# Optimization experiments

Hardware: AMD Instinct MI355X
Metric: run time of the kernel (lower is better)

## Reference

```python
import jax, jax.numpy as jnp
import numpy as np

N = 8192
F_IN, F1, F2 = 11, 16, 32
HEADS = 3
D_CAT = 2 * F2          # 64, concat of interface + neighborhood branches
D_POOL = D_CAT * HEADS  # 192


def setup_inputs() -> dict:
    key = jax.random.key(0)
    ks = jax.random.split(key, 16)
    s = 0.1
    return {
        "x_int": jax.random.normal(ks[0], (N, F_IN), jnp.float32),
        "x_nh": jax.random.normal(ks[1], (N, F_IN), jnp.float32),
        # dense soft adjacencies, scaled ~1/N so aggregates stay O(1)
        "adj_int": jax.random.uniform(ks[2], (N, N), jnp.float32) / N,
        "adj_nh": jax.random.uniform(ks[3], (N, N), jnp.float32) / N,
        "W1_int": jax.random.normal(ks[4], (F_IN, F1), jnp.float32) * s,
        "b1_int": jnp.zeros((F1,), jnp.float32),
        "W1_nh": jax.random.normal(ks[5], (F_IN, F1), jnp.float32) * s,
        "b1_nh": jnp.zeros((F1,), jnp.float32),
        "W2_int": jax.random.normal(ks[6], (F1, F2), jnp.float32) * s,
        "b2_int": jnp.zeros((F2,), jnp.float32),
        "W2_nh": jax.random.normal(ks[7], (F1, F2), jnp.float32) * s,
        "b2_nh": jnp.zeros((F2,), jnp.float32),
        "W_att": jax.random.normal(ks[8], (D_CAT, HEADS), jnp.float32) * s,
        "W_dense": jax.random.normal(ks[9], (D_POOL, 1), jnp.float32) * s,
        "b_dense": jnp.zeros((1,), jnp.float32),
    }


def _dgcn(A, x, W, b):
    # diffusion graph conv: aggregate neighbors then linear + relu
    return jax.nn.relu(A @ (x @ W) + b)


def reference(x_int, x_nh, adj_int, adj_nh,
              W1_int, b1_int, W1_nh, b1_nh,
              W2_int, b2_int, W2_nh, b2_nh,
              W_att, W_dense, b_dense):
    # conv1 / conv2, two parallel graph branches
    h_int = _dgcn(adj_int, x_int, W1_int, b1_int)   # [N, 16]
    h_nh = _dgcn(adj_nh, x_nh, W1_nh, b1_nh)        # [N, 16]
    h_int = _dgcn(adj_int, h_int, W2_int, b2_int)   # [N, 32]
    h_nh = _dgcn(adj_nh, h_nh, W2_nh, b2_nh)        # [N, 32]
    h = jnp.concatenate([h_int, h_nh], axis=1)      # [N, 64]
    # multi-head tanh self-attention pooling over nodes
    scores = jnp.tanh(h @ W_att)                    # [N, heads]
    att = jax.nn.softmax(scores, axis=0)            # softmax over nodes
    pooled = jnp.einsum('nh,nd->hd', att, h).reshape(1, D_POOL)  # [1, 192]
    out = pooled @ W_dense + b_dense                # [1, 1]
    return jnp.squeeze(out, 1)                      # [1]
```

## Files before the change

kernel.cpp:

```cpp
#include <hip/hip_runtime.h>


constexpr int N = 8192;

__global__ void k_dense_in(const float* __restrict__ x0, const float* __restrict__ x1,
                           const float* __restrict__ W0, const float* __restrict__ W1,
                           float* __restrict__ o0, float* __restrict__ o1) {
    const int branch = blockIdx.y;
    const float* __restrict__ x = branch ? x1 : x0;
    const float* __restrict__ W = branch ? W1 : W0;
    float* __restrict__ o = branch ? o1 : o0;
    __shared__ float sW[11 * 16];
    if (threadIdx.x < 176) sW[threadIdx.x] = W[threadIdx.x];
    __syncthreads();
    const int n = blockIdx.x * blockDim.x + threadIdx.x;
    float xr[11];
#pragma unroll
    for (int j = 0; j < 11; ++j) xr[j] = x[n * 11 + j];
    float acc[16];
#pragma unroll
    for (int f = 0; f < 16; ++f) acc[f] = 0.f;
#pragma unroll
    for (int j = 0; j < 11; ++j)
#pragma unroll
        for (int f = 0; f < 16; ++f) acc[f] += xr[j] * sW[j * 16 + f];
#pragma unroll
    for (int f = 0; f < 16; ++f) o[f * N + n] = acc[f];
}

__global__ void k_dense_mid(const float* __restrict__ h0, const float* __restrict__ h1,
                            const float* __restrict__ W0, const float* __restrict__ W1,
                            float* __restrict__ o0, float* __restrict__ o1) {
    const int branch = blockIdx.y;
    const float* __restrict__ h = branch ? h1 : h0;
    const float* __restrict__ W = branch ? W1 : W0;
    float* __restrict__ o = branch ? o1 : o0;
    __shared__ float sW[16 * 32];
    for (int i = threadIdx.x; i < 512; i += blockDim.x) sW[i] = W[i];
    __syncthreads();
    const int n = blockIdx.x * blockDim.x + threadIdx.x;
    float hr[16];
#pragma unroll
    for (int q = 0; q < 4; ++q)
        *reinterpret_cast<float4*>(&hr[q * 4]) =
            *reinterpret_cast<const float4*>(&h[n * 16 + q * 4]);
    float acc[32];
#pragma unroll
    for (int f = 0; f < 32; ++f) acc[f] = 0.f;
#pragma unroll
    for (int j = 0; j < 16; ++j)
#pragma unroll
        for (int f = 0; f < 32; ++f) acc[f] += hr[j] * sW[j * 32 + f];
#pragma unroll
    for (int f = 0; f < 32; ++f) o[f * N + n] = acc[f];
}

template <int F>
__global__ __launch_bounds__(512, 2) void k_spmm(
    const float* __restrict__ A, const float* __restrict__ PT,
    float* __restrict__ pb) {
    constexpr int W = 512;
    constexpr int NS = N / W;
    constexpr int C = 2;
    constexpr int FS = F / 16;
    constexpr int G = (F == 16) ? 2 : 4;

    __shared__ float plds[F * W];

    const int tid = threadIdx.x, lane = tid & 63, w = tid >> 6;
    const int quad = w / FS;
    const int f0 = (w % FS) * 16;
    const int rb = blockIdx.x / NS, sl = blockIdx.x % NS;
    const int K0 = sl * W;
    const int row0 = rb * 64 + quad * 4 * G;

    const float* __restrict__ Ab = A + (size_t)row0 * N + K0 + 4 * lane;

    float4 a[4][C];
    auto loadG = [&](int g) {
#pragma unroll
        for (int r = 0; r < 4; ++r)
#pragma unroll
            for (int c = 0; c < C; ++c)
                a[r][c] = *reinterpret_cast<const float4*>(
                    Ab + (size_t)(g * 4 + r) * N + c * 256);
    };

    loadG(0);

    constexpr int NF4 = F * W / 4;
    for (int i = tid; i < NF4; i += 512) {
        const int fl = i / (W / 4), k4 = i % (W / 4);
        *reinterpret_cast<float4*>(&plds[fl * W + 4 * k4]) =
            *reinterpret_cast<const float4*>(PT + (size_t)fl * N + K0 + 4 * k4);
    }
    __syncthreads();

    for (int g = 0; g < G; ++g) {
        float acc[4][16];
#pragma unroll
        for (int r = 0; r < 4; ++r)
#pragma unroll
            for (int f = 0; f < 16; ++f) acc[r][f] = 0.f;

#pragma unroll
        for (int c = 0; c < C; ++c)
#pragma unroll
            for (int f = 0; f < 16; ++f) {
                const float4 pv = *reinterpret_cast<const float4*>(
                    &plds[(f0 + f) * W + c * 256 + 4 * lane]);
#pragma unroll
                for (int r = 0; r < 4; ++r) {
                    acc[r][f] += a[r][c].x * pv.x;
                    acc[r][f] += a[r][c].y * pv.y;
                    acc[r][f] += a[r][c].z * pv.z;
                    acc[r][f] += a[r][c].w * pv.w;
                }
            }

        if (g + 1 < G) loadG(g + 1);

        float red[4];
#pragma unroll
        for (int r = 0; r < 4; ++r) {
            float v[16];
#pragma unroll
            for (int i = 0; i < 16; ++i) v[i] = acc[r][i];
#pragma unroll
            for (int s = 0; s < 4; ++s) {
                const int bit = (lane >> s) & 1;
#pragma unroll
                for (int i = 0; i < (16 >> s); i += 2) {
                    const float t0 = __shfl_xor(v[i], 1 << s);
                    const float t1 = __shfl_xor(v[i + 1], 1 << s);
                    v[i >> 1] = bit ? (v[i + 1] + t1) : (v[i] + t0);
                }
            }
            float rs = v[0];
            rs += __shfl_xor(rs, 16);
            rs += __shfl_xor(rs, 32);
            red[r] = rs;
        }
        const int rsel = lane >> 4;
        const float val = rsel == 0 ? red[0] : rsel == 1 ? red[1] : rsel == 2 ? red[2] : red[3];
        pb[((size_t)sl * N + row0 + g * 4 + rsel) * F + f0 + (lane & 15)] = val;
    }
}

template <int F, int NS>
__global__ void k_reduce(const float* __restrict__ pb, const float* __restrict__ bias,
                         float* __restrict__ o, int ostride) {
    const int i = blockIdx.x * 256 + threadIdx.x;
    const int r = i / F, f = i % F;
    float s = bias[f];
#pragma unroll
    for (int sl = 0; sl < NS; ++sl) s += pb[(size_t)sl * N * F + i];
    o[(size_t)r * ostride + f] = fmaxf(s, 0.f);
}

__global__ void k_att_pool(const float* __restrict__ h, const float* __restrict__ Watt,
                           const float* __restrict__ Wd, float* __restrict__ partials) {
    __shared__ float sWa[64 * 3];
    __shared__ float sWd[192];
    for (int i = threadIdx.x; i < 192; i += blockDim.x) {
        sWa[i] = Watt[i];
        sWd[i] = Wd[i];
    }
    __syncthreads();
    const int n = blockIdx.x * blockDim.x + threadIdx.x;
    float hv[64];
#pragma unroll
    for (int q = 0; q < 16; ++q)
        *reinterpret_cast<float4*>(&hv[q * 4]) =
            *reinterpret_cast<const float4*>(&h[(size_t)n * 64 + q * 4]);
    float s0 = 0.f, s1 = 0.f, s2 = 0.f;
#pragma unroll
    for (int d = 0; d < 64; ++d) {
        s0 += hv[d] * sWa[d * 3 + 0];
        s1 += hv[d] * sWa[d * 3 + 1];
        s2 += hv[d] * sWa[d * 3 + 2];
    }
    float dot0 = 0.f, dot1 = 0.f, dot2 = 0.f;
#pragma unroll
    for (int d = 0; d < 64; ++d) {
        dot0 += hv[d] * sWd[0 * 64 + d];
        dot1 += hv[d] * sWd[1 * 64 + d];
        dot2 += hv[d] * sWd[2 * 64 + d];
    }
    const float e0 = expf(tanhf(s0));
    const float e1 = expf(tanhf(s1));
    const float e2 = expf(tanhf(s2));
    float vals[6] = {e0, e1, e2, e0 * dot0, e1 * dot1, e2 * dot2};
#pragma unroll
    for (int i = 0; i < 6; ++i) {
        float v = vals[i];
#pragma unroll
        for (int off = 1; off < 64; off <<= 1) v += __shfl_xor(v, off);
        vals[i] = v;
    }
    __shared__ float sred[4][6];
    const int wave = threadIdx.x >> 6, lane = threadIdx.x & 63;
    if (lane == 0) {
#pragma unroll
        for (int i = 0; i < 6; ++i) sred[wave][i] = vals[i];
    }
    __syncthreads();
    if (threadIdx.x == 0) {
#pragma unroll
        for (int i = 0; i < 6; ++i)
            partials[blockIdx.x * 6 + i] = sred[0][i] + sred[1][i] + sred[2][i] + sred[3][i];
    }
}

__global__ void k_att_final(const float* __restrict__ partials, const float* __restrict__ bd,
                            float* __restrict__ out) {
    if (threadIdx.x == 0) {
        float Z0 = 0.f, Z1 = 0.f, Z2 = 0.f, U0 = 0.f, U1 = 0.f, U2 = 0.f;
        for (int b = 0; b < 32; ++b) {
            Z0 += partials[b * 6 + 0];
            Z1 += partials[b * 6 + 1];
            Z2 += partials[b * 6 + 2];
            U0 += partials[b * 6 + 3];
            U1 += partials[b * 6 + 4];
            U2 += partials[b * 6 + 5];
        }
        out[0] = U0 / Z0 + U1 / Z1 + U2 / Z2 + bd[0];
    }
}

extern "C" void kernel_launch(void* const* d_in, const int* in_sizes, int n_in,
                              void* d_out, int out_size, void* d_ws, size_t ws_size,
                              hipStream_t stream) {
    const float* x_int   = (const float*)d_in[0];
    const float* x_nh    = (const float*)d_in[1];
    const float* adj_int = (const float*)d_in[2];
    const float* adj_nh  = (const float*)d_in[3];
    const float* W1_int  = (const float*)d_in[4];
    const float* b1_int  = (const float*)d_in[5];
    const float* W1_nh   = (const float*)d_in[6];
    const float* b1_nh   = (const float*)d_in[7];
    const float* W2_int  = (const float*)d_in[8];
    const float* b2_int  = (const float*)d_in[9];
    const float* W2_nh   = (const float*)d_in[10];
    const float* b2_nh   = (const float*)d_in[11];
    const float* W_att   = (const float*)d_in[12];
    const float* W_dense = (const float*)d_in[13];
    const float* b_dense = (const float*)d_in[14];

    float* ws = (float*)d_ws;
    float* P1T_0 = ws;
    float* P1T_1 = ws + 131072;
    float* H1_0  = ws + 262144;
    float* H1_1  = ws + 393216;
    float* P2T_0 = ws + 524288;
    float* P2T_1 = ws + 786432;
    float* hcat  = ws + 1048576;
    float* attp  = ws + 1572864;
    float* part  = ws + 1573120;
    float* out = (float*)d_out;

    k_dense_in<<<dim3(32, 2), 256, 0, stream>>>(x_int, x_nh, W1_int, W1_nh, P1T_0, P1T_1);
    k_spmm<16><<<2048, 512, 0, stream>>>(adj_int, P1T_0, part);
    k_reduce<16, 16><<<512, 256, 0, stream>>>(part, b1_int, H1_0, 16);
    k_spmm<16><<<2048, 512, 0, stream>>>(adj_nh, P1T_1, part);
    k_reduce<16, 16><<<512, 256, 0, stream>>>(part, b1_nh, H1_1, 16);
    k_dense_mid<<<dim3(32, 2), 256, 0, stream>>>(H1_0, H1_1, W2_int, W2_nh, P2T_0, P2T_1);
    k_spmm<32><<<2048, 512, 0, stream>>>(adj_int, P2T_0, part);
    k_reduce<32, 16><<<1024, 256, 0, stream>>>(part, b2_int, hcat, 64);
    k_spmm<32><<<2048, 512, 0, stream>>>(adj_nh, P2T_1, part);
    k_reduce<32, 16><<<1024, 256, 0, stream>>>(part, b2_nh, hcat + 32, 64);
    k_att_pool<<<32, 256, 0, stream>>>(hcat, W_att, W_dense, attp);
    k_att_final<<<1, 64, 0, stream>>>(attp, b_dense, out);
}
```

Before: 613.3 us.

## Drop split-K partials: full-K per block, fuse bias+ReLU, merge branch launches

The dense adjacency matmul kernel no longer splits K into 16 slices writing partial sums. Each block now loops over all K windows with an 8-row register tile, restages the P tile in shared memory every window, and applies bias and ReLU directly in its epilogue. This removes the separate reduce kernels and the partial-buffer traffic, and both graph branches run in one launch via blockIdx.y. The costs are far fewer blocks (256 or 512 instead of 2048 per branch), which may underfill the GPU, more registers for the 8x16 accumulators, and two barriers per window with little overlap between staging and compute.

```diff
diff --git a/kernel.cpp b/kernel.cpp
--- a/kernel.cpp
+++ b/kernel.cpp
@@ -57,72 +57,92 @@
 
 template <int F>
 __global__ __launch_bounds__(512, 2) void k_spmm(
-    const float* __restrict__ A, const float* __restrict__ PT,
-    float* __restrict__ pb) {
+    const float* __restrict__ A0, const float* __restrict__ A1,
+    const float* __restrict__ PT0, const float* __restrict__ PT1,
+    const float* __restrict__ b0, const float* __restrict__ b1,
+    float* __restrict__ o0, float* __restrict__ o1,
+    int ostride, int ooff) {
     constexpr int W = 512;
-    constexpr int NS = N / W;
-    constexpr int C = 2;
+    constexpr int NWIN = N / W;
     constexpr int FS = F / 16;
-    constexpr int G = (F == 16) ? 2 : 4;
+    constexpr int RPB = (F == 16) ? 64 : 32;
 
     __shared__ float plds[F * W];
 
     const int tid = threadIdx.x, lane = tid & 63, w = tid >> 6;
-    const int quad = w / FS;
+    const int rset = w / FS;
     const int f0 = (w % FS) * 16;
-    const int rb = blockIdx.x / NS, sl = blockIdx.x % NS;
-    const int K0 = sl * W;
-    const int row0 = rb * 64 + quad * 4 * G;
-
-    const float* __restrict__ Ab = A + (size_t)row0 * N + K0 + 4 * lane;
-
-    float4 a[4][C];
-    auto loadG = [&](int g) {
-#pragma unroll
-        for (int r = 0; r < 4; ++r)
-#pragma unroll
-            for (int c = 0; c < C; ++c)
+    const int br = blockIdx.y;
+    const float* __restrict__ A = br ? A1 : A0;
+    const float* __restrict__ PT = br ? PT1 : PT0;
+    const float* __restrict__ bias = br ? b1 : b0;
+    float* __restrict__ o = (br ? o1 : o0) + ooff * br;
+
+    const int row0 = blockIdx.x * RPB + rset * 8;
+    const float* __restrict__ Ab = A + (size_t)row0 * N + 4 * lane;
+
+    float4 a[8][2];
+    auto loadA = [&](int t) {
+        const int K0 = t * W;
+#pragma unroll
+        for (int r = 0; r < 8; ++r)
+#pragma unroll
+            for (int c = 0; c < 2; ++c)
                 a[r][c] = *reinterpret_cast<const float4*>(
-                    Ab + (size_t)(g * 4 + r) * N + c * 256);
+                    Ab + (size_t)r * N + K0 + c * 256);
     };
 
-    loadG(0);
-
-    constexpr int NF4 = F * W / 4;
-    for (int i = tid; i < NF4; i += 512) {
-        const int fl = i / (W / 4), k4 = i % (W / 4);
-        *reinterpret_cast<float4*>(&plds[fl * W + 4 * k4]) =
-            *reinterpret_cast<const float4*>(PT + (size_t)fl * N + K0 + 4 * k4);
-    }
-    __syncthreads();
-
-    for (int g = 0; g < G; ++g) {
-        float acc[4][16];
-#pragma unroll
-        for (int r = 0; r < 4; ++r)
-#pragma unroll
-            for (int f = 0; f < 16; ++f) acc[r][f] = 0.f;
-
-#pragma unroll
-        for (int c = 0; c < C; ++c)
+    auto stageP = [&](int t) {
+        const int K0 = t * W;
+        constexpr int NF4 = F * W / 4;
+        for (int i = tid; i < NF4; i += 512) {
+            const int fl = i / (W / 4), k4 = i % (W / 4);
+            *reinterpret_cast<float4*>(&plds[fl * W + 4 * k4]) =
+                *reinterpret_cast<const float4*>(PT + (size_t)fl * N + K0 + 4 * k4);
+        }
+    };
+
+    float acc[8][16];
+#pragma unroll
+    for (int r = 0; r < 8; ++r)
+#pragma unroll
+        for (int f = 0; f < 16; ++f) acc[r][f] = 0.f;
+
+    loadA(0);
+    stageP(0);
+    __syncthreads();
+
+    for (int t = 0; t < NWIN; ++t) {
+#pragma unroll
+        for (int c = 0; c < 2; ++c)
 #pragma unroll
             for (int f = 0; f < 16; ++f) {
                 const float4 pv = *reinterpret_cast<const float4*>(
                     &plds[(f0 + f) * W + c * 256 + 4 * lane]);
 #pragma unroll
-                for (int r = 0; r < 4; ++r) {
+                for (int r = 0; r < 8; ++r) {
                     acc[r][f] += a[r][c].x * pv.x;
                     acc[r][f] += a[r][c].y * pv.y;
                     acc[r][f] += a[r][c].z * pv.z;
                     acc[r][f] += a[r][c].w * pv.w;
                 }
             }
-
-        if (g + 1 < G) loadG(g + 1);
-
+        if (t + 1 < NWIN) loadA(t + 1);
+        __syncthreads();
+        if (t + 1 < NWIN) {
+            stageP(t + 1);
+            __syncthreads();
+        }
+    }
+
+    const float bv = bias[f0 + (lane & 15)];
+    const int rsel = lane >> 4;
+#pragma unroll
+    for (int h = 0; h < 2; ++h) {
         float red[4];
 #pragma unroll
-        for (int r = 0; r < 4; ++r) {
+        for (int r4 = 0; r4 < 4; ++r4) {
+            const int r = h * 4 + r4;
             float v[16];
 #pragma unroll
             for (int i = 0; i < 16; ++i) v[i] = acc[r][i];
@@ -139,23 +159,12 @@
             float rs = v[0];
             rs += __shfl_xor(rs, 16);
             rs += __shfl_xor(rs, 32);
-            red[r] = rs;
-        }
-        const int rsel = lane >> 4;
+            red[r4] = rs;
+        }
         const float val = rsel == 0 ? red[0] : rsel == 1 ? red[1] : rsel == 2 ? red[2] : red[3];
-        pb[((size_t)sl * N + row0 + g * 4 + rsel) * F + f0 + (lane & 15)] = val;
-    }
-}
-
-template <int F, int NS>
-__global__ void k_reduce(const float* __restrict__ pb, const float* __restrict__ bias,
-                         float* __restrict__ o, int ostride) {
-    const int i = blockIdx.x * 256 + threadIdx.x;
-    const int r = i / F, f = i % F;
-    float s = bias[f];
-#pragma unroll
-    for (int sl = 0; sl < NS; ++sl) s += pb[(size_t)sl * N * F + i];
-    o[(size_t)r * ostride + f] = fmaxf(s, 0.f);
+        o[(size_t)(row0 + h * 4 + rsel) * ostride + f0 + (lane & 15)] =
+            fmaxf(val + bv, 0.f);
+    }
 }
 
 __global__ void k_att_pool(const float* __restrict__ h, const float* __restrict__ Watt,
@@ -256,19 +265,14 @@
     float* P2T_1 = ws + 786432;
     float* hcat  = ws + 1048576;
     float* attp  = ws + 1572864;
-    float* part  = ws + 1573120;
     float* out = (float*)d_out;
 
     k_dense_in<<<dim3(32, 2), 256, 0, stream>>>(x_int, x_nh, W1_int, W1_nh, P1T_0, P1T_1);
-    k_spmm<16><<<2048, 512, 0, stream>>>(adj_int, P1T_0, part);
-    k_reduce<16, 16><<<512, 256, 0, stream>>>(part, b1_int, H1_0, 16);
-    k_spmm<16><<<2048, 512, 0, stream>>>(adj_nh, P1T_1, part);
-    k_reduce<16, 16><<<512, 256, 0, stream>>>(part, b1_nh, H1_1, 16);
+    k_spmm<16><<<dim3(128, 2), 512, 0, stream>>>(adj_int, adj_nh, P1T_0, P1T_1,
+                                                 b1_int, b1_nh, H1_0, H1_1, 16, 0);
     k_dense_mid<<<dim3(32, 2), 256, 0, stream>>>(H1_0, H1_1, W2_int, W2_nh, P2T_0, P2T_1);
-    k_spmm<32><<<2048, 512, 0, stream>>>(adj_int, P2T_0, part);
-    k_reduce<32, 16><<<1024, 256, 0, stream>>>(part, b2_int, hcat, 64);
-    k_spmm<32><<<2048, 512, 0, stream>>>(adj_nh, P2T_1, part);
-    k_reduce<32, 16><<<1024, 256, 0, stream>>>(part, b2_nh, hcat + 32, 64);
+    k_spmm<32><<<dim3(256, 2), 512, 0, stream>>>(adj_int, adj_nh, P2T_0, P2T_1,
+                                                 b2_int, b2_nh, hcat, hcat, 64, 32);
     k_att_pool<<<32, 256, 0, stream>>>(hcat, W_att, W_dense, attp);
     k_att_final<<<1, 64, 0, stream>>>(attp, b_dense, out);
 }
```

After: 1.764 ms. 2.88x slower.
